# Kernel optimization log

Hardware: AMD Instinct MI355X
Metric: run time of the kernel (lower is better)

The kernel has to match this reference:

```python
import jax, jax.numpy as jnp
import numpy as np

VOCAB, E, U, T, B = 32000, 256, 512, 512, 128

def setup_inputs() -> dict:
    key = jax.random.key(0)
    ks = jax.random.split(key, 12)
    s = lambda k, shape, scale: jax.random.normal(k, shape, dtype=jnp.float32) * scale
    return {
        "sentence": jax.random.randint(ks[0], (B, T), 0, VOCAB, dtype=jnp.int32),
        "emb": s(ks[1], (VOCAB, E), 0.05),
        "Wx": s(ks[2], (E, 4 * U), 1.0 / np.sqrt(E)),   # input->gates (i,f,g,o)
        "Wh": s(ks[3], (U, 4 * U), 1.0 / np.sqrt(U)),   # hidden->gates
        "b":  jnp.zeros((4 * U,), dtype=jnp.float32),
        "W1": s(ks[4], (U, 128), 1.0 / np.sqrt(U)),
        "b1": jnp.zeros((128,), dtype=jnp.float32),
        "W2": s(ks[5], (128, 64), 1.0 / np.sqrt(128)),
        "b2": jnp.zeros((64,), dtype=jnp.float32),
        "W3": s(ks[6], (64, 1), 1.0 / np.sqrt(64)),
        "b3": jnp.zeros((1,), dtype=jnp.float32),
    }

def reference(sentence, emb, Wx, Wh, b, W1, b1, W2, b2, W3, b3):
    # Embedding lookup: [B, T, E]
    x = emb[sentence]
    batch = x.shape[0]
    units = Wh.shape[0]
    h0 = jnp.zeros((batch, units), dtype=x.dtype)
    c0 = jnp.zeros((batch, units), dtype=x.dtype)

    def step(carry, xt):
        h, c = carry
        z = xt @ Wx + h @ Wh + b                      # [B, 4U]
        i, f, g, o = jnp.split(z, 4, axis=-1)
        i = jax.nn.sigmoid(i)
        f = jax.nn.sigmoid(f)
        g = jnp.tanh(g)
        o = jax.nn.sigmoid(o)
        c_new = f * c + i * g
        h_new = o * jnp.tanh(c_new)
        return (h_new, c_new), None

    (h, _), _ = jax.lax.scan(step, (h0, c0), jnp.swapaxes(x, 0, 1))  # scan over T
    h1 = jax.nn.relu(h @ W1 + b1)
    h2 = jax.nn.relu(h1 @ W2 + b2)
    return jax.nn.sigmoid(h2 @ W3 + b3)               # [B, 1]
```

## Files before the change

kernel.cpp:

```cpp
#include <hip/hip_runtime.h>
#include <hip/hip_bf16.h>
#include <hip/hip_fp16.h>


#define B_ 128
#define T_ 512
#define E_ 256
#define U_ 512
#define NWG_ 128
#define HROW_ 516

typedef __attribute__((ext_vector_type(4))) _Float16 half4;
typedef __attribute__((ext_vector_type(4))) float floatx4;
typedef unsigned long long u64t;
typedef unsigned int u32t;

#define MFMA16 __builtin_amdgcn_mfma_f32_16x16x16f16

__device__ __forceinline__ float sigmf(float x) { return 1.0f / (1.0f + __expf(-x)); }
__device__ __forceinline__ float tanh_f(float x) { return 2.0f / (1.0f + __expf(-2.0f * x)) - 1.0f; }

__global__ void prep_x_kernel(const int* __restrict__ sent,
                              const float* __restrict__ emb,
                              _Float16* __restrict__ X) {
  int gid = blockIdx.x * blockDim.x + threadIdx.x;
  int e8 = gid & 31;
  int row = gid >> 5;
  int b = row & 127;
  int t = row >> 7;
  int word = sent[b * T_ + t];
  const float* src = emb + (size_t)word * E_ + e8 * 8;
  float4 v0 = *(const float4*)(src);
  float4 v1 = *(const float4*)(src + 4);
  _Float16 o[8] = {(_Float16)v0.x, (_Float16)v0.y, (_Float16)v0.z, (_Float16)v0.w,
                   (_Float16)v1.x, (_Float16)v1.y, (_Float16)v1.z, (_Float16)v1.w};
  _Float16* dst = X + (size_t)row * E_ + e8 * 8;
  *(half4*)dst = *(half4*)o;
  *(half4*)(dst + 4) = *(half4*)(o + 4);
}

__global__ __launch_bounds__(512, 1) void lstm_kernel(
    const _Float16* __restrict__ X,
    const float* __restrict__ Wx, const float* __restrict__ Wh,
    const float* __restrict__ bias,
    _Float16* __restrict__ Hq, u32t* FlagA, u32t* FlagB, u32t* XccTab) {
  __shared__ __align__(16) char smem[98304];
  _Float16* Hs = (_Float16*)smem;
  float* Rs = (float*)(smem + 16512);
  u32t* xl = (u32t*)(smem + 24704);
  volatile u32t* goP = (volatile u32t*)(smem + 25216);
  u32t* pcntP = (u32t*)(smem + 25220);

  const int bid = blockIdx.x;
  const int d = bid & 7;
  const int s = bid >> 3;
  const int tid = threadIdx.x;
  const int lane = tid & 63;
  const int wave = tid >> 6;
  const int p16 = lane & 15;
  const int quad = lane >> 4;
  const int sg = wave & 3;
  const int kh = wave >> 2;

  if (tid == 0) {
    *goP = 0u;
    *pcntP = 0u;
    u32t myx = (u32t)__builtin_amdgcn_s_getreg(63508) & 0xFFu;
    __hip_atomic_store(XccTab + bid, 0x5A5A0000u | myx, __ATOMIC_RELAXED,
                       __HIP_MEMORY_SCOPE_AGENT);
  }
  if (wave == 0) {
    u32t v0, v1;
    for (;;) {
      v0 = __hip_atomic_load(XccTab + lane, __ATOMIC_RELAXED,
                             __HIP_MEMORY_SCOPE_AGENT);
      v1 = __hip_atomic_load(XccTab + 64 + lane, __ATOMIC_RELAXED,
                             __HIP_MEMORY_SCOPE_AGENT);
      if (__all(((v0 >> 16) == 0x5A5Au) & ((v1 >> 16) == 0x5A5Au))) break;
      __builtin_amdgcn_s_sleep(8);
    }
    xl[lane] = v0;
    xl[lane + 64] = v1;
  }
  __syncthreads();
  int fastv;
  {
    const u32t ref = xl[d];
    bool dom = true;
    for (int j = 1; j < 16; ++j) dom = dom && (xl[d + 8 * j] == ref);
    bool sane = false;
    const u32t z0 = xl[0];
    for (int e = 1; e < 128; ++e) sane = sane || (xl[e] != z0);
    fastv = (dom && sane) ? 1 : 0;
  }
  const bool fastp = (bool)__builtin_amdgcn_readfirstlane(fastv);

  const int C0 = ((p16 >> 3) & 1) * 512 + s * 32 + sg * 8 + (p16 & 7);
  const int C1 = C0 + 1024;
  half4 b0r[32], b1r[32];
  if (kh == 0) {
#pragma unroll
    for (int i = 0; i < 16; ++i) {
      int kb = 16 + i;
#pragma unroll
      for (int j = 0; j < 4; ++j) {
        int gk = kb * 16 + quad * 4 + j;
        b0r[i][j] = (_Float16)Wh[(size_t)(gk - E_) * 2048 + C0];
        b1r[i][j] = (_Float16)Wh[(size_t)(gk - E_) * 2048 + C1];
      }
    }
  } else {
#pragma unroll
    for (int i = 0; i < 32; ++i) {
      int kb = (i < 16) ? i : (16 + i);
#pragma unroll
      for (int j = 0; j < 4; ++j) {
        int gk = kb * 16 + quad * 4 + j;
        float w0 = (gk < E_) ? Wx[(size_t)gk * 2048 + C0]
                             : Wh[(size_t)(gk - E_) * 2048 + C0];
        float w1 = (gk < E_) ? Wx[(size_t)gk * 2048 + C1]
                             : Wh[(size_t)(gk - E_) * 2048 + C1];
        b0r[i][j] = (_Float16)w0;
        b1r[i][j] = (_Float16)w1;
      }
    }
  }

  const int u0 = s * 32 + sg * 8 + (quad & 1) * 4;
  const floatx4 bi = *(const floatx4*)(bias + u0);
  const floatx4 bf = *(const floatx4*)(bias + 512 + u0);
  const floatx4 bg = *(const floatx4*)(bias + 1024 + u0);
  const floatx4 bo = *(const floatx4*)(bias + 1536 + u0);

  float cst[4] = {0.f, 0.f, 0.f, 0.f};

  const int brow = d * 16 + p16;
  const int ko = quad * 4;

  for (int t = 0; t < T_; ++t) {
    const int pin = t & 1, pout = pin ^ 1;

    floatx4 acc0 = {0.f, 0.f, 0.f, 0.f};
    floatx4 acc1 = {0.f, 0.f, 0.f, 0.f};

    if (kh == 1) {
      const _Float16* xr = X + ((size_t)t * B_ + brow) * E_ + ko;
#pragma unroll
      for (int i = 0; i < 16; ++i) {
        half4 a = *(const half4*)(xr + i * 16);
        acc0 = MFMA16(b0r[i], a, acc0, 0, 0, 0);
        acc1 = MFMA16(b1r[i], a, acc1, 0, 0, 0);
      }
    } else if (t > 0) {
      const u32t tgt = (u32t)t;
      if (wave == 0) {
        u32t v;
        if (fastp) {
          u32t* fa = FlagA + (size_t)(pin * 8 + d) * 16;
          const u32t* fb = FlagB + (size_t)(pin * 8 + d) * 16;
          int budget = 512;
          for (;;) {
            if (budget > 0) {
              u32t old = tgt;
              if (lane < 16) {
                u32t* ap = fa + lane;
                asm volatile(
                    "global_atomic_add %0, %1, %2, off sc0\n\t"
                    "s_waitcnt vmcnt(0)"
                    : "=&v"(old) : "v"(ap), "v"(0u) : "memory");
              }
              v = old;
            } else {
              v = (lane < 16)
                      ? __hip_atomic_load(fb + lane, __ATOMIC_RELAXED,
                                          __HIP_MEMORY_SCOPE_AGENT)
                      : tgt;
            }
            if (__all(v == tgt)) break;
            --budget;
            if (budget < 500) __builtin_amdgcn_s_sleep(1);
          }
        } else {
          const u32t* fb = FlagB + (size_t)(pin * 8 + d) * 16;
          for (;;) {
            v = (lane < 16)
                    ? __hip_atomic_load(fb + lane, __ATOMIC_RELAXED,
                                        __HIP_MEMORY_SCOPE_AGENT)
                    : tgt;
            if (__all(v == tgt)) break;
            __builtin_amdgcn_s_sleep(1);
          }
        }
        if (lane == 0) *goP = tgt;
      } else {
        u32t g;
        do { g = *goP; } while (g < tgt);
      }

      const _Float16* hq = Hq + ((size_t)(pin * 8 + d) * 16 + wave * 4) * 512;
      u64t hv[8];
      if (fastp) {
        const u64t* hqb = (const u64t*)hq + lane;
        u64t h0, h1, h2, h3, h4, h5, h6, h7;
        asm volatile(
            "global_load_dwordx2 %0, %8, off sc0\n\t"
            "global_load_dwordx2 %1, %8, off offset:512 sc0\n\t"
            "global_load_dwordx2 %2, %8, off offset:1024 sc0\n\t"
            "global_load_dwordx2 %3, %8, off offset:1536 sc0\n\t"
            "global_load_dwordx2 %4, %8, off offset:2048 sc0\n\t"
            "global_load_dwordx2 %5, %8, off offset:2560 sc0\n\t"
            "global_load_dwordx2 %6, %8, off offset:3072 sc0\n\t"
            "global_load_dwordx2 %7, %8, off offset:3584 sc0\n\t"
            "s_waitcnt vmcnt(0)"
            : "=&v"(h0), "=&v"(h1), "=&v"(h2), "=&v"(h3),
              "=&v"(h4), "=&v"(h5), "=&v"(h6), "=&v"(h7)
            : "v"(hqb)
            : "memory");
        hv[0] = h0; hv[1] = h1; hv[2] = h2; hv[3] = h3;
        hv[4] = h4; hv[5] = h5; hv[6] = h6; hv[7] = h7;
      } else {
#pragma unroll
        for (int j = 0; j < 8; ++j) {
          size_t idx = (size_t)(j >> 1) * 128 + (j & 1) * 64 + lane;
          hv[j] = __hip_atomic_load((const u64t*)hq + idx, __ATOMIC_RELAXED,
                                    __HIP_MEMORY_SCOPE_AGENT);
        }
      }
#pragma unroll
      for (int j = 0; j < 8; ++j) {
        int r = wave * 4 + (j >> 1), half = j & 1;
        *(u64t*)(Hs + r * HROW_ + half * 256 + lane * 4) = hv[j];
      }
    }
    __syncthreads();

    if (t > 0) {
#pragma unroll
      for (int i = 0; i < 16; ++i) {
        int hk = kh * 16 + i;
        half4 a = *(const half4*)(Hs + p16 * HROW_ + hk * 16 + ko);
        const int wi = (kh == 0) ? i : (16 + i);
        acc0 = MFMA16(b0r[wi], a, acc0, 0, 0, 0);
        acc1 = MFMA16(b1r[wi], a, acc1, 0, 0, 0);
      }
    }

    if (kh == 1) {
      float* wb = Rs + sg * 512;
      *(floatx4*)(wb + lane * 4) = acc0;
      *(floatx4*)(wb + 256 + lane * 4) = acc1;
    }
    __syncthreads();

    if (kh == 0) {
      const float* rb = Rs + sg * 512;
      floatx4 z0v = acc0 + *(const floatx4*)(rb + lane * 4);
      floatx4 z1v = acc1 + *(const floatx4*)(rb + 256 + lane * 4);
      half4 hp4;
#pragma unroll
      for (int r = 0; r < 4; ++r) {
        float fraw = __shfl_xor(z0v[r], 32, 64);
        float oraw = __shfl_xor(z1v[r], 32, 64);
        float iv = sigmf(z0v[r] + bi[r]);
        float gv = tanh_f(z1v[r] + bg[r]);
        float fv = sigmf(fraw + bf[r]);
        float ov = sigmf(oraw + bo[r]);
        float cn = fv * cst[r] + iv * gv;
        cst[r] = cn;
        hp4[r] = (_Float16)(ov * tanh_f(cn));
      }
      if (quad < 2) {
        u64t pk = __builtin_bit_cast(u64t, hp4);
        u64t* hp =
            (u64t*)(Hq + ((size_t)(pout * 8 + d) * 16 + p16) * 512 + u0);
        if (fastp) {
          *hp = pk;
        } else {
          __hip_atomic_store(hp, pk, __ATOMIC_RELAXED,
                             __HIP_MEMORY_SCOPE_AGENT);
        }
      }

      asm volatile("s_waitcnt vmcnt(0)" ::: "memory");
      __builtin_amdgcn_sched_barrier(0);
      if (lane == 0) {
        u32t old = atomicAdd(pcntP, 1u);
        if (old == (u32t)(4 * t + 3)) {
          size_t fo = (size_t)(pout * 8 + d) * 16 + s;
          if (fastp) {
            u32t* ap = FlagA + fo;
            u32t nv = (u32t)(t + 1);
            asm volatile("global_atomic_swap %0, %1, off"
                         :: "v"(ap), "v"(nv) : "memory");
          }
          __hip_atomic_store(FlagB + fo, (u32t)(t + 1), __ATOMIC_RELAXED,
                             __HIP_MEMORY_SCOPE_AGENT);
        }
      }
    }
  }
}

__global__ void head_kernel(const _Float16* __restrict__ Hq,
                            const float* __restrict__ W1, const float* __restrict__ b1,
                            const float* __restrict__ W2, const float* __restrict__ b2,
                            const float* __restrict__ W3, const float* __restrict__ b3,
                            float* __restrict__ out) {
  __shared__ float hs[512];
  __shared__ float h1[128];
  __shared__ float h2[64];
  int row = blockIdx.x;
  int tid = threadIdx.x;
  int dd = row >> 4, rr = row & 15;
  const _Float16* hrow = Hq + ((size_t)dd * 16 + rr) * 512;
  for (int k = tid; k < 512; k += 128) hs[k] = (float)hrow[k];
  __syncthreads();
  float a = b1[tid];
  for (int k = 0; k < 512; ++k) a += hs[k] * W1[k * 128 + tid];
  h1[tid] = fmaxf(a, 0.0f);
  __syncthreads();
  if (tid < 64) {
    float a2 = b2[tid];
    for (int k = 0; k < 128; ++k) a2 += h1[k] * W2[k * 64 + tid];
    h2[tid] = fmaxf(a2, 0.0f);
  }
  __syncthreads();
  if (tid == 0) {
    float a3 = b3[0];
    for (int k = 0; k < 64; ++k) a3 += h2[k] * W3[k];
    out[row] = 1.0f / (1.0f + __expf(-a3));
  }
}

extern "C" void kernel_launch(void* const* d_in, const int* in_sizes, int n_in,
                              void* d_out, int out_size, void* d_ws, size_t ws_size,
                              hipStream_t stream) {
  const int* sent = (const int*)d_in[0];
  const float* emb = (const float*)d_in[1];
  const float* Wx = (const float*)d_in[2];
  const float* Wh = (const float*)d_in[3];
  const float* b = (const float*)d_in[4];
  const float* W1 = (const float*)d_in[5];
  const float* b1 = (const float*)d_in[6];
  const float* W2 = (const float*)d_in[7];
  const float* b2 = (const float*)d_in[8];
  const float* W3 = (const float*)d_in[9];
  const float* b3 = (const float*)d_in[10];
  float* out = (float*)d_out;

  char* ws = (char*)d_ws;
  _Float16* X = (_Float16*)(ws);
  _Float16* Hq = (_Float16*)(ws + (size_t)33554432);
  u32t* FlagA = (u32t*)(ws + (size_t)33554432 + 262144);
  u32t* FlagB = (u32t*)(ws + (size_t)33554432 + 263168);
  u32t* XccTab = (u32t*)(ws + (size_t)33554432 + 264192);

  hipMemsetAsync(FlagA, 0, 2560, stream);
  prep_x_kernel<<<8192, 256, 0, stream>>>(sent, emb, X);
  lstm_kernel<<<NWG_, 512, 0, stream>>>(X, Wx, Wh, b, Hq, FlagA, FlagB, XccTab);
  head_kernel<<<128, 128, 0, stream>>>(Hq, W1, b1, W2, b2, W3, b3, out);
}
```

Before: 1.776 ms.

## Replace per-slice flag array with single atomic counter per group in LSTM step sync

Cross-workgroup synchronization between timesteps now uses one counter per group and parity, incremented by each of the 16 producer slices, instead of 16 separate flags polled by 16 lanes. A single lane polls that counter until it reaches the cumulative target, which cuts polling traffic from 16 atomics per iteration to one. The spin budget is raised, and the other waves now also poll the shared go-flag. A dependency offset taken from the go value is added to the load address, and it is always zero for realistic step counts.

```diff
diff --git a/kernel.cpp b/kernel.cpp
--- a/kernel.cpp
+++ b/kernel.cpp
@@ -153,51 +153,44 @@
       }
     } else if (t > 0) {
       const u32t tgt = (u32t)t;
-      if (wave == 0) {
+      const u32t target = 16u * (((u32t)t + 1u) >> 1);
+      if (wave == 0 && lane == 0) {
         u32t v;
         if (fastp) {
-          u32t* fa = FlagA + (size_t)(pin * 8 + d) * 16;
+          u32t* ap = FlagA + (size_t)(pin * 8 + d) * 16;
           const u32t* fb = FlagB + (size_t)(pin * 8 + d) * 16;
-          int budget = 512;
+          int budget = 4096;
           for (;;) {
             if (budget > 0) {
-              u32t old = tgt;
-              if (lane < 16) {
-                u32t* ap = fa + lane;
-                asm volatile(
-                    "global_atomic_add %0, %1, %2, off sc0\n\t"
-                    "s_waitcnt vmcnt(0)"
-                    : "=&v"(old) : "v"(ap), "v"(0u) : "memory");
-              }
-              v = old;
+              asm volatile(
+                  "global_atomic_add %0, %1, %2, off sc0\n\t"
+                  "s_waitcnt vmcnt(0)"
+                  : "=&v"(v) : "v"(ap), "v"(0u) : "memory");
             } else {
-              v = (lane < 16)
-                      ? __hip_atomic_load(fb + lane, __ATOMIC_RELAXED,
-                                          __HIP_MEMORY_SCOPE_AGENT)
-                      : tgt;
+              v = __hip_atomic_load(fb, __ATOMIC_RELAXED,
+                                    __HIP_MEMORY_SCOPE_AGENT);
+              __builtin_amdgcn_s_sleep(1);
             }
-            if (__all(v == tgt)) break;
+            if (v >= target) break;
             --budget;
-            if (budget < 500) __builtin_amdgcn_s_sleep(1);
           }
         } else {
           const u32t* fb = FlagB + (size_t)(pin * 8 + d) * 16;
           for (;;) {
-            v = (lane < 16)
-                    ? __hip_atomic_load(fb + lane, __ATOMIC_RELAXED,
-                                        __HIP_MEMORY_SCOPE_AGENT)
-                    : tgt;
-            if (__all(v == tgt)) break;
+            v = __hip_atomic_load(fb, __ATOMIC_RELAXED,
+                                  __HIP_MEMORY_SCOPE_AGENT);
+            if (v >= target) break;
             __builtin_amdgcn_s_sleep(1);
           }
         }
-        if (lane == 0) *goP = tgt;
-      } else {
-        u32t g;
-        do { g = *goP; } while (g < tgt);
-      }
-
-      const _Float16* hq = Hq + ((size_t)(pin * 8 + d) * 16 + wave * 4) * 512;
+        *goP = tgt;
+      }
+      u32t g;
+      do { g = *goP; } while (g < tgt);
+      const size_t dep = (size_t)(g >> 16);
+
+      const _Float16* hq =
+          Hq + ((size_t)(pin * 8 + d) * 16 + wave * 4) * 512 + dep;
       u64t hv[8];
       if (fastp) {
         const u64t* hqb = (const u64t*)hq + lane;
@@ -286,15 +279,14 @@
       if (lane == 0) {
         u32t old = atomicAdd(pcntP, 1u);
         if (old == (u32t)(4 * t + 3)) {
-          size_t fo = (size_t)(pout * 8 + d) * 16 + s;
+          size_t fo = (size_t)(pout * 8 + d) * 16;
           if (fastp) {
             u32t* ap = FlagA + fo;
-            u32t nv = (u32t)(t + 1);
-            asm volatile("global_atomic_swap %0, %1, off"
-                         :: "v"(ap), "v"(nv) : "memory");
+            asm volatile("global_atomic_add %0, %1, off"
+                         :: "v"(ap), "v"(1u) : "memory");
           }
-          __hip_atomic_store(FlagB + fo, (u32t)(t + 1), __ATOMIC_RELAXED,
-                             __HIP_MEMORY_SCOPE_AGENT);
+          __hip_atomic_fetch_add(FlagB + fo, 1u, __ATOMIC_RELAXED,
+                                 __HIP_MEMORY_SCOPE_AGENT);
         }
       }
     }
```

New measurement: 1.800 ms. No clear change (+1.4%).
